# Kernel optimization log

Measured on AMD Instinct MI355X. Metric: run time of the kernel, lower is better.

Reference implementation:

```python
import jax, jax.numpy as jnp
import numpy as np

V, D = 100000, 128
B, Q, C, T = 1024, 64, 64, 8


def setup_inputs() -> dict:
    key = jax.random.key(0)
    ks = jax.random.split(key, 9)
    embed = jax.random.normal(ks[0], (V, D), dtype=jnp.float32) * 0.1
    embed = embed.at[0].set(0.0)  # padding_idx=0
    q_ids = jax.random.randint(ks[1], (B, Q), 1, V)
    c_ids = jax.random.randint(ks[2], (B, C, T), 1, V)
    num_qs = jax.random.randint(ks[3], (B,), 1, Q + 1)
    num_cols = jax.random.randint(ks[4], (B,), 1, C + 1)
    W_h = jax.random.normal(ks[5], (5 * D, D), dtype=jnp.float32) * 0.02
    b_h = jnp.zeros((D,), jnp.float32)
    W_o = jax.random.normal(ks[6], (D, 1), dtype=jnp.float32) * 0.02
    b_o = jnp.zeros((1,), jnp.float32)
    return {"q_ids": q_ids, "c_ids": c_ids, "num_qs": num_qs, "num_cols": num_cols,
            "embed": embed, "W_h": W_h, "b_h": b_h, "W_o": W_o, "b_o": b_o}


def _forward(q_ids, c_ids, num_qs, num_cols, embed, W_h, b_h, W_o, b_o):
    d = embed.shape[1]
    # ColumnSummarizer: pad-masked mean over column tokens -> [B, C, D]
    c_tok = embed[c_ids]                       # [B, C, T, D]
    c_mask = (c_ids != 0).astype(c_tok.dtype)  # [B, C, T]
    denom = jnp.maximum(c_mask.sum(-1, keepdims=True), 1.0)
    c_h = (c_tok * c_mask[..., None]).sum(-2) / denom  # [B, C, D]
    # QuestionSummarizer: q_h = token embeddings, q_summary = length-masked mean
    q_h = embed[q_ids]                         # [B, Q, D]
    q_valid = (jnp.arange(q_h.shape[1])[None, :] < num_qs[:, None])  # [B, Q]
    qv = q_valid.astype(q_h.dtype)
    q_summary = (q_h * qv[..., None]).sum(1) / jnp.maximum(
        num_qs[:, None].astype(q_h.dtype), 1.0)  # [B, D]
    # scaled dot-product attention, columns attend over question tokens
    sim = jnp.einsum('bcd,bqd->bcq', c_h, q_h) / jnp.sqrt(jnp.asarray(d, c_h.dtype))
    sim = jnp.where(q_valid[:, None, :], sim, -jnp.inf)  # mask padded q tokens
    att = jax.nn.softmax(sim, axis=-1)                    # [B, C, Q]
    weighted_q = jnp.einsum('bcq,bqd->bcd', att, q_h)     # [B, C, D]
    q_tiled = jnp.broadcast_to(q_summary[:, None, :], c_h.shape)
    feats = jnp.concatenate(
        [q_tiled, c_h, weighted_q, c_h * weighted_q, jnp.abs(c_h - weighted_q)],
        axis=-1)                                           # [B, C, 5D]
    h = jnp.tanh(feats @ W_h + b_h)
    return h @ W_o + b_o                                   # [B, C, 1]


def reference(q_ids, c_ids, num_qs, num_cols, embed, W_h, b_h, W_o, b_o):
    return _forward(q_ids, c_ids, num_qs, num_cols, embed, W_h, b_h, W_o, b_o)
```

## Files before the change

kernel.cpp:

```cpp
#include <hip/hip_runtime.h>


typedef __attribute__((ext_vector_type(8))) short     short8;
typedef __attribute__((ext_vector_type(8))) __bf16    bf16x8;
typedef __attribute__((ext_vector_type(4))) float     f32x4;
typedef __attribute__((ext_vector_type(4))) int       int4v;

#define SWZ8(row, off) ((off) ^ (((row) & 7) << 4))
#define SWZQ(row, off) ((off) ^ (((row) & 7) << 4) ^ ((((row) >> 3) & 3) << 5))

#define A_CH   0
#define A_QH   16384
#define A_LDS  32768

#define CH_OFF  0
#define QH_OFF  16384
#define X_OFF   32768
#define LDS_SIZE 40960

__device__ __forceinline__ unsigned short f2bf(float x) {
    __bf16 h = (__bf16)x;
    return __builtin_bit_cast(unsigned short, h);
}
__device__ __forceinline__ float bf2f(unsigned short u) {
    return __builtin_bit_cast(float, ((unsigned)u) << 16);
}
__device__ __forceinline__ float bflo(unsigned u) {
    return __builtin_bit_cast(float, u << 16);
}
__device__ __forceinline__ float bfhi(unsigned u) {
    return __builtin_bit_cast(float, u & 0xFFFF0000u);
}
__device__ __forceinline__ unsigned pk2(float a, float b) {
    return (unsigned)f2bf(a) | ((unsigned)f2bf(b) << 16);
}
__device__ __forceinline__ f32x4 mfma16(short8 a, short8 b, f32x4 c) {
    return __builtin_amdgcn_mfma_f32_16x16x32_bf16(
        __builtin_bit_cast(bf16x8, a), __builtin_bit_cast(bf16x8, b), c, 0, 0, 0);
}

__global__ __launch_bounds__(256) void el_prep(const float* __restrict__ W_h,
                                               unsigned short* __restrict__ whT) {
    int t = blockIdx.x * 256 + threadIdx.x;
    int k = t >> 7, n = t & 127;
    whT[n * 640 + k] = f2bf(W_h[t]);
}

__global__ __launch_bounds__(256) void el_conv(const float* __restrict__ e,
                                               unsigned short* __restrict__ ebf) {
    long i = ((long)blockIdx.x * 256 + threadIdx.x) * 8;
    f32x4 a = *(const f32x4*)(e + i);
    f32x4 c = *(const f32x4*)(e + i + 4);
    uint4 pk;
    pk.x = pk2(a[0], a[1]); pk.y = pk2(a[2], a[3]);
    pk.z = pk2(c[0], c[1]); pk.w = pk2(c[2], c[3]);
    *(uint4*)(ebf + i) = pk;
}

__global__ __launch_bounds__(256, 4) void el_main_a(
    const int* __restrict__ q_ids, const int* __restrict__ c_ids,
    const int* __restrict__ num_qs,
    const unsigned short* __restrict__ ebf,
    const unsigned short* __restrict__ whT,
    unsigned short* __restrict__ qsum_ws,
    unsigned short* __restrict__ att_ws,
    const float* __restrict__ b_h,
    const float* __restrict__ W_o, const float* __restrict__ b_o,
    float* __restrict__ out)
{
    __shared__ __align__(16) char smem[A_LDS];
    const int tid = threadIdx.x;
    const int b = blockIdx.x;
    const int nq = num_qs[b] > 0 ? num_qs[b] : 1;
    unsigned short* batt = att_ws + (size_t)b * 4096;
    float* bqp = (float*)batt;

    if (tid < 64) out[(b << 6) + tid] = b_o[0];

    {
        const int l4 = tid & 15, gg = tid >> 4;
        #pragma unroll 2
        for (int cc = 0; cc < 4; ++cc) {
            const int c = gg + cc * 16;
            const int* idp = c_ids + (((b << 6) + c) << 3);
            int4v i0 = *(const int4v*)idp, i1 = *(const int4v*)(idp + 4);
            int id8[8] = {i0[0], i0[1], i0[2], i0[3], i1[0], i1[1], i1[2], i1[3]};
            int cnt = 0;
            #pragma unroll
            for (int t = 0; t < 8; ++t) cnt += (id8[t] != 0);
            float acc[8] = {0.f,0.f,0.f,0.f,0.f,0.f,0.f,0.f};
            #pragma unroll
            for (int t = 0; t < 8; ++t) {
                uint4 v = *(const uint4*)(ebf + (long)id8[t] * 128 + l4 * 8);
                acc[0] += bflo(v.x); acc[1] += bfhi(v.x);
                acc[2] += bflo(v.y); acc[3] += bfhi(v.y);
                acc[4] += bflo(v.z); acc[5] += bfhi(v.z);
                acc[6] += bflo(v.w); acc[7] += bfhi(v.w);
            }
            float inv = 1.0f / (float)(cnt > 0 ? cnt : 1);
            uint4 pk;
            pk.x = pk2(acc[0]*inv, acc[1]*inv); pk.y = pk2(acc[2]*inv, acc[3]*inv);
            pk.z = pk2(acc[4]*inv, acc[5]*inv); pk.w = pk2(acc[6]*inv, acc[7]*inv);
            *(uint4*)(smem + A_CH + SWZ8(c, c * 256 + l4 * 16)) = pk;
        }
        float qa[8] = {0.f,0.f,0.f,0.f,0.f,0.f,0.f,0.f};
        #pragma unroll
        for (int qq = 0; qq < 4; ++qq) {
            const int q = gg + (qq << 4);
            int id = q_ids[(b << 6) + q];
            uint4 v = *(const uint4*)(ebf + (long)id * 128 + l4 * 8);
            *(uint4*)(smem + A_QH + SWZQ(q, q * 256 + l4 * 16)) = v;
            if (q < nq) {
                qa[0] += bflo(v.x); qa[1] += bfhi(v.x);
                qa[2] += bflo(v.y); qa[3] += bfhi(v.y);
                qa[4] += bflo(v.z); qa[5] += bfhi(v.z);
                qa[6] += bflo(v.w); qa[7] += bfhi(v.w);
            }
        }
        #pragma unroll
        for (int e = 0; e < 8; ++e) {
            qa[e] += __shfl_xor(qa[e], 16);
            qa[e] += __shfl_xor(qa[e], 32);
        }
        const int lane = tid & 63, w = tid >> 6;
        if (lane < 16) {
            *(f32x4*)(bqp + w * 128 + lane * 8)     = (f32x4){qa[0],qa[1],qa[2],qa[3]};
            *(f32x4*)(bqp + w * 128 + lane * 8 + 4) = (f32x4){qa[4],qa[5],qa[6],qa[7]};
        }
    }
    __syncthreads();

    if (tid < 128) {
        float s = bqp[tid] + bqp[128 + tid] + bqp[256 + tid] + bqp[384 + tid];
        qsum_ws[(b << 7) + tid] = f2bf(s / (float)nq);
    }
    __syncthreads();

    const int lane = tid & 63, w = tid >> 6;
    const int lr = lane & 15, lg = lane >> 4;

    {
        short8 a[4];
        const int arow = w * 16 + lr;
        #pragma unroll
        for (int s = 0; s < 4; ++s)
            a[s] = *(const short8*)(smem + A_CH + SWZ8(arow, arow * 256 + s * 64 + lg * 16));
        f32x4 sim[4];
        #pragma unroll
        for (int ct = 0; ct < 4; ++ct) {
            f32x4 acc = {0.f, 0.f, 0.f, 0.f};
            const int q = ct * 16 + lr;
            #pragma unroll
            for (int s = 0; s < 4; ++s) {
                short8 bf = *(const short8*)(smem + A_QH + SWZQ(q, q * 256 + s * 64 + lg * 16));
                acc = mfma16(a[s], bf, acc);
            }
            sim[ct] = acc;
        }
        const float scale = 0.08838834764831845f;
        #pragma unroll
        for (int ct = 0; ct < 4; ++ct) {
            const int q = ct * 16 + lr;
            #pragma unroll
            for (int r = 0; r < 4; ++r)
                sim[ct][r] = (q < nq) ? sim[ct][r] * scale : -3.0e38f;
        }
        float mx[4], sm[4];
        #pragma unroll
        for (int r = 0; r < 4; ++r)
            mx[r] = fmaxf(fmaxf(sim[0][r], sim[1][r]), fmaxf(sim[2][r], sim[3][r]));
        #pragma unroll
        for (int off = 1; off <= 8; off <<= 1)
            #pragma unroll
            for (int r = 0; r < 4; ++r)
                mx[r] = fmaxf(mx[r], __shfl_xor(mx[r], off));
        #pragma unroll
        for (int ct = 0; ct < 4; ++ct)
            #pragma unroll
            for (int r = 0; r < 4; ++r)
                sim[ct][r] = __expf(sim[ct][r] - mx[r]);
        #pragma unroll
        for (int r = 0; r < 4; ++r)
            sm[r] = (sim[0][r] + sim[1][r]) + (sim[2][r] + sim[3][r]);
        #pragma unroll
        for (int off = 1; off <= 8; off <<= 1)
            #pragma unroll
            for (int r = 0; r < 4; ++r)
                sm[r] += __shfl_xor(sm[r], off);
        const int cbase = w * 16 + lg * 4;
        #pragma unroll
        for (int ct = 0; ct < 4; ++ct)
            #pragma unroll
            for (int r = 0; r < 4; ++r) {
                int c = cbase + r, q = ct * 16 + lr;
                batt[c * 64 + q] = f2bf(sim[ct][r] * (1.0f / sm[r]));
            }
    }
    __syncthreads();

    f32x4 wqa[8];
    {
        short8 pa[2];
        const int prow = w * 16 + lr;
        #pragma unroll
        for (int s = 0; s < 2; ++s)
            pa[s] = *(const short8*)(batt + prow * 64 + s * 32 + lg * 8);
        #pragma unroll
        for (int ct = 0; ct < 8; ++ct) {
            f32x4 acc = {0.f, 0.f, 0.f, 0.f};
            const int d = ct * 16 + lr;
            const int dlx = (d << 1) ^ (lg << 5);
            #pragma unroll
            for (int s = 0; s < 2; ++s) {
                const int qbase = (s << 5) + (lg << 3);
                short8 bf;
                #pragma unroll
                for (int j = 0; j < 8; ++j) {
                    int off = A_QH + ((qbase + j) << 8) + (dlx ^ (j << 4));
                    bf[j] = *(const short*)(smem + off);
                }
                acc = mfma16(pa[s], bf, acc);
            }
            wqa[ct] = acc;
        }
    }
    __syncthreads();
    {
        const int cbase = w * 16 + lg * 4;
        #pragma unroll
        for (int ct = 0; ct < 8; ++ct)
            #pragma unroll
            for (int r = 0; r < 4; ++r) {
                int c = cbase + r, d = ct * 16 + lr;
                *(unsigned short*)(smem + A_QH + SWZQ(c, c * 256 + d * 2)) =
                    f2bf(wqa[ct][r]);
            }
    }
    __syncthreads();

    {
        f32x4 acc[4][2];
        #pragma unroll
        for (int rt = 0; rt < 4; ++rt) {
            acc[rt][0] = (f32x4){0.f, 0.f, 0.f, 0.f};
            acc[rt][1] = (f32x4){0.f, 0.f, 0.f, 0.f};
        }
        const int n0 = w * 32 + lr, n1 = n0 + 16;
        const int klane = lg * 8;
        short8 qsf[4];
        #pragma unroll
        for (int sk = 0; sk < 4; ++sk)
            qsf[sk] = *(const short8*)(qsum_ws + (b << 7) + sk * 32 + klane);
        const float bh0 = b_h[n0], bh1 = b_h[n1];
        const float wo0 = W_o[n0], wo1 = W_o[n1];

        for (int sk = 0; sk < 4; ++sk) {
            short8 B0[5], B1[5];
            #pragma unroll
            for (int p = 0; p < 5; ++p) {
                B0[p] = *(const short8*)(whT + n0 * 640 + p * 128 + sk * 32 + klane);
                B1[p] = *(const short8*)(whT + n1 * 640 + p * 128 + sk * 32 + klane);
            }
            #pragma unroll
            for (int rt = 0; rt < 4; ++rt) {
                const int row = rt * 16 + lr;
                short8 chf = *(const short8*)(smem + A_CH + SWZ8(row, row * 256 + sk * 64 + lg * 16));
                short8 wqf = *(const short8*)(smem + A_QH + SWZQ(row, row * 256 + sk * 64 + lg * 16));
                short8 prf, adf;
                #pragma unroll
                for (int e = 0; e < 8; ++e) {
                    float cv = bf2f((unsigned short)chf[e]);
                    float wv = bf2f((unsigned short)wqf[e]);
                    prf[e] = (short)f2bf(cv * wv);
                    adf[e] = (short)f2bf(fabsf(cv - wv));
                }
                acc[rt][0] = mfma16(qsf[sk], B0[0], acc[rt][0]);
                acc[rt][1] = mfma16(qsf[sk], B1[0], acc[rt][1]);
                acc[rt][0] = mfma16(chf,     B0[1], acc[rt][0]);
                acc[rt][1] = mfma16(chf,     B1[1], acc[rt][1]);
                acc[rt][0] = mfma16(wqf,     B0[2], acc[rt][0]);
                acc[rt][1] = mfma16(wqf,     B1[2], acc[rt][1]);
                acc[rt][0] = mfma16(prf,     B0[3], acc[rt][0]);
                acc[rt][1] = mfma16(prf,     B1[3], acc[rt][1]);
                acc[rt][0] = mfma16(adf,     B0[4], acc[rt][0]);
                acc[rt][1] = mfma16(adf,     B1[4], acc[rt][1]);
            }
        }

        #pragma unroll
        for (int rt = 0; rt < 4; ++rt)
            #pragma unroll
            for (int r = 0; r < 4; ++r) {
                float x0 = acc[rt][0][r] + bh0;
                float x1 = acc[rt][1][r] + bh1;
                float t0 = 1.0f - 2.0f / (__expf(2.0f * x0) + 1.0f);
                float t1 = 1.0f - 2.0f / (__expf(2.0f * x1) + 1.0f);
                float po = t0 * wo0 + t1 * wo1;
                #pragma unroll
                for (int off = 1; off <= 8; off <<= 1)
                    po += __shfl_xor(po, off);
                if (lr == 0)
                    atomicAdd(out + (b << 6) + rt * 16 + lg * 4 + r, po);
            }
    }
}

template <bool BF16E>
__global__ __launch_bounds__(256, 4) void el_main_b(
    const int* __restrict__ q_ids, const int* __restrict__ c_ids,
    const int* __restrict__ num_qs, const float* __restrict__ emb,
    const unsigned short* __restrict__ ebf,
    const unsigned short* __restrict__ whT,
    unsigned short* __restrict__ qsum_ws,
    const float* __restrict__ b_h,
    const float* __restrict__ W_o, const float* __restrict__ b_o,
    float* __restrict__ out)
{
    __shared__ __align__(16) char smem[LDS_SIZE];
    const int tid = threadIdx.x;
    const int b = blockIdx.x;
    const int nq = num_qs[b] > 0 ? num_qs[b] : 1;

    {
        const int l4 = tid & 15, gg = tid >> 4;
        #pragma unroll 2
        for (int cc = 0; cc < 4; ++cc) {
            const int c = gg + cc * 16;
            const int* idp = c_ids + (((b << 6) + c) << 3);
            int4v i0 = *(const int4v*)idp, i1 = *(const int4v*)(idp + 4);
            int id8[8] = {i0[0], i0[1], i0[2], i0[3], i1[0], i1[1], i1[2], i1[3]};
            int cnt = 0;
            #pragma unroll
            for (int t = 0; t < 8; ++t) cnt += (id8[t] != 0);
            float acc[8] = {0.f,0.f,0.f,0.f,0.f,0.f,0.f,0.f};
            #pragma unroll
            for (int t = 0; t < 8; ++t) {
                if constexpr (BF16E) {
                    uint4 v = *(const uint4*)(ebf + (long)id8[t] * 128 + l4 * 8);
                    acc[0] += bflo(v.x); acc[1] += bfhi(v.x);
                    acc[2] += bflo(v.y); acc[3] += bfhi(v.y);
                    acc[4] += bflo(v.z); acc[5] += bfhi(v.z);
                    acc[6] += bflo(v.w); acc[7] += bfhi(v.w);
                } else {
                    f32x4 lo = *(const f32x4*)(emb + (long)id8[t] * 128 + l4 * 8);
                    f32x4 hi = *(const f32x4*)(emb + (long)id8[t] * 128 + l4 * 8 + 4);
                    acc[0] += lo[0]; acc[1] += lo[1]; acc[2] += lo[2]; acc[3] += lo[3];
                    acc[4] += hi[0]; acc[5] += hi[1]; acc[6] += hi[2]; acc[7] += hi[3];
                }
            }
            float inv = 1.0f / (float)(cnt > 0 ? cnt : 1);
            uint4 pk;
            pk.x = pk2(acc[0]*inv, acc[1]*inv); pk.y = pk2(acc[2]*inv, acc[3]*inv);
            pk.z = pk2(acc[4]*inv, acc[5]*inv); pk.w = pk2(acc[6]*inv, acc[7]*inv);
            *(uint4*)(smem + CH_OFF + SWZ8(c, c * 256 + l4 * 16)) = pk;
        }
        float qa[8] = {0.f,0.f,0.f,0.f,0.f,0.f,0.f,0.f};
        #pragma unroll
        for (int qq = 0; qq < 4; ++qq) {
            const int q = gg + (qq << 4);
            int id = q_ids[(b << 6) + q];
            uint4 v;
            if constexpr (BF16E) {
                v = *(const uint4*)(ebf + (long)id * 128 + l4 * 8);
            } else {
                f32x4 lo = *(const f32x4*)(emb + (long)id * 128 + l4 * 8);
                f32x4 hi = *(const f32x4*)(emb + (long)id * 128 + l4 * 8 + 4);
                v.x = pk2(lo[0], lo[1]); v.y = pk2(lo[2], lo[3]);
                v.z = pk2(hi[0], hi[1]); v.w = pk2(hi[2], hi[3]);
            }
            *(uint4*)(smem + QH_OFF + SWZQ(q, q * 256 + l4 * 16)) = v;
            if (q < nq) {
                qa[0] += bflo(v.x); qa[1] += bfhi(v.x);
                qa[2] += bflo(v.y); qa[3] += bfhi(v.y);
                qa[4] += bflo(v.z); qa[5] += bfhi(v.z);
                qa[6] += bflo(v.w); qa[7] += bfhi(v.w);
            }
        }
        float* qsp = (float*)(smem + X_OFF);
        *(f32x4*)(qsp + gg * 128 + l4 * 8)     = (f32x4){qa[0], qa[1], qa[2], qa[3]};
        *(f32x4*)(qsp + gg * 128 + l4 * 8 + 4) = (f32x4){qa[4], qa[5], qa[6], qa[7]};
    }
    __syncthreads();

    if (tid < 128) {
        const float* qsp = (const float*)(smem + X_OFF);
        float s = 0.f;
        #pragma unroll
        for (int g = 0; g < 16; ++g) s += qsp[g * 128 + tid];
        qsum_ws[(b << 7) + tid] = f2bf(s / (float)nq);
    }
    __syncthreads();

    const int lane = tid & 63, w = tid >> 6;
    const int lr = lane & 15, lg = lane >> 4;

    {
        short8 a[4];
        const int arow = w * 16 + lr;
        #pragma unroll
        for (int s = 0; s < 4; ++s)
            a[s] = *(const short8*)(smem + CH_OFF + SWZ8(arow, arow * 256 + s * 64 + lg * 16));
        f32x4 sim[4];
        #pragma unroll
        for (int ct = 0; ct < 4; ++ct) {
            f32x4 acc = {0.f, 0.f, 0.f, 0.f};
            const int q = ct * 16 + lr;
            #pragma unroll
            for (int s = 0; s < 4; ++s) {
                short8 bf = *(const short8*)(smem + QH_OFF + SWZQ(q, q * 256 + s * 64 + lg * 16));
                acc = mfma16(a[s], bf, acc);
            }
            sim[ct] = acc;
        }
        const float scale = 0.08838834764831845f;
        #pragma unroll
        for (int ct = 0; ct < 4; ++ct) {
            const int q = ct * 16 + lr;
            #pragma unroll
            for (int r = 0; r < 4; ++r)
                sim[ct][r] = (q < nq) ? sim[ct][r] * scale : -3.0e38f;
        }
        float mx[4], sm[4];
        #pragma unroll
        for (int r = 0; r < 4; ++r)
            mx[r] = fmaxf(fmaxf(sim[0][r], sim[1][r]), fmaxf(sim[2][r], sim[3][r]));
        #pragma unroll
        for (int off = 1; off <= 8; off <<= 1)
            #pragma unroll
            for (int r = 0; r < 4; ++r)
                mx[r] = fmaxf(mx[r], __shfl_xor(mx[r], off));
        #pragma unroll
        for (int ct = 0; ct < 4; ++ct)
            #pragma unroll
            for (int r = 0; r < 4; ++r)
                sim[ct][r] = __expf(sim[ct][r] - mx[r]);
        #pragma unroll
        for (int r = 0; r < 4; ++r)
            sm[r] = (sim[0][r] + sim[1][r]) + (sim[2][r] + sim[3][r]);
        #pragma unroll
        for (int off = 1; off <= 8; off <<= 1)
            #pragma unroll
            for (int r = 0; r < 4; ++r)
                sm[r] += __shfl_xor(sm[r], off);
        const int cbase = w * 16 + lg * 4;
        #pragma unroll
        for (int ct = 0; ct < 4; ++ct)
            #pragma unroll
            for (int r = 0; r < 4; ++r) {
                int c = cbase + r, q = ct * 16 + lr;
                *(unsigned short*)(smem + X_OFF + SWZ8(c, c * 128 + q * 2)) =
                    f2bf(sim[ct][r] * (1.0f / sm[r]));
            }
    }
    __syncthreads();

    f32x4 wqa[8];
    {
        short8 pa[2];
        const int arow = w * 16 + lr;
        #pragma unroll
        for (int s = 0; s < 2; ++s)
            pa[s] = *(const short8*)(smem + X_OFF + SWZ8(arow, arow * 128 + s * 64 + lg * 16));
        #pragma unroll
        for (int ct = 0; ct < 8; ++ct) {
            f32x4 acc = {0.f, 0.f, 0.f, 0.f};
            const int d = ct * 16 + lr;
            const int dlx = (d << 1) ^ (lg << 5);
            #pragma unroll
            for (int s = 0; s < 2; ++s) {
                const int qbase = (s << 5) + (lg << 3);
                short8 bf;
                #pragma unroll
                for (int j = 0; j < 8; ++j) {
                    int off = QH_OFF + ((qbase + j) << 8) + (dlx ^ (j << 4));
                    bf[j] = *(const short*)(smem + off);
                }
                acc = mfma16(pa[s], bf, acc);
            }
            wqa[ct] = acc;
        }
    }
    __syncthreads();
    {
        const int cbase = w * 16 + lg * 4;
        #pragma unroll
        for (int ct = 0; ct < 8; ++ct)
            #pragma unroll
            for (int r = 0; r < 4; ++r) {
                int c = cbase + r, d = ct * 16 + lr;
                *(unsigned short*)(smem + QH_OFF + SWZQ(c, c * 256 + d * 2)) =
                    f2bf(wqa[ct][r]);
            }
    }
    __syncthreads();

    {
        f32x4 acc[4][2];
        #pragma unroll
        for (int rt = 0; rt < 4; ++rt) {
            acc[rt][0] = (f32x4){0.f, 0.f, 0.f, 0.f};
            acc[rt][1] = (f32x4){0.f, 0.f, 0.f, 0.f};
        }
        const int n0 = w * 32 + lr, n1 = n0 + 16;
        const int klane = lg * 8;
        short8 qsf[4];
        #pragma unroll
        for (int sk = 0; sk < 4; ++sk)
            qsf[sk] = *(const short8*)(qsum_ws + (b << 7) + sk * 32 + klane);
        const float bh0 = b_h[n0], bh1 = b_h[n1];
        const float wo0 = W_o[n0], wo1 = W_o[n1];

        for (int sk = 0; sk < 4; ++sk) {
            short8 B0[5], B1[5];
            #pragma unroll
            for (int p = 0; p < 5; ++p) {
                B0[p] = *(const short8*)(whT + n0 * 640 + p * 128 + sk * 32 + klane);
                B1[p] = *(const short8*)(whT + n1 * 640 + p * 128 + sk * 32 + klane);
            }
            #pragma unroll
            for (int rt = 0; rt < 4; ++rt) {
                const int row = rt * 16 + lr;
                short8 chf = *(const short8*)(smem + CH_OFF + SWZ8(row, row * 256 + sk * 64 + lg * 16));
                short8 wqf = *(const short8*)(smem + QH_OFF + SWZQ(row, row * 256 + sk * 64 + lg * 16));
                short8 prf, adf;
                #pragma unroll
                for (int e = 0; e < 8; ++e) {
                    float cv = bf2f((unsigned short)chf[e]);
                    float wv = bf2f((unsigned short)wqf[e]);
                    prf[e] = (short)f2bf(cv * wv);
                    adf[e] = (short)f2bf(fabsf(cv - wv));
                }
                acc[rt][0] = mfma16(qsf[sk], B0[0], acc[rt][0]);
                acc[rt][1] = mfma16(qsf[sk], B1[0], acc[rt][1]);
                acc[rt][0] = mfma16(chf,     B0[1], acc[rt][0]);
                acc[rt][1] = mfma16(chf,     B1[1], acc[rt][1]);
                acc[rt][0] = mfma16(wqf,     B0[2], acc[rt][0]);
                acc[rt][1] = mfma16(wqf,     B1[2], acc[rt][1]);
                acc[rt][0] = mfma16(prf,     B0[3], acc[rt][0]);
                acc[rt][1] = mfma16(prf,     B1[3], acc[rt][1]);
                acc[rt][0] = mfma16(adf,     B0[4], acc[rt][0]);
                acc[rt][1] = mfma16(adf,     B1[4], acc[rt][1]);
            }
        }

        #pragma unroll
        for (int rt = 0; rt < 4; ++rt)
            #pragma unroll
            for (int r = 0; r < 4; ++r) {
                float x0 = acc[rt][0][r] + bh0;
                float x1 = acc[rt][1][r] + bh1;
                float t0 = 1.0f - 2.0f / (__expf(2.0f * x0) + 1.0f);
                float t1 = 1.0f - 2.0f / (__expf(2.0f * x1) + 1.0f);
                float po = t0 * wo0 + t1 * wo1;
                #pragma unroll
                for (int off = 1; off <= 8; off <<= 1)
                    po += __shfl_xor(po, off);
                if (lr == 0)
                    *(float*)(smem + X_OFF + (w * 64 + rt * 16 + lg * 4 + r) * 4) = po;
            }
    }
    __syncthreads();

    if (tid < 64) {
        float o = b_o[0];
        #pragma unroll
        for (int w2 = 0; w2 < 4; ++w2)
            o += *(const float*)(smem + X_OFF + (w2 * 64 + tid) * 4);
        out[(b << 6) + tid] = o;
    }
}

extern "C" void kernel_launch(void* const* d_in, const int* in_sizes, int n_in,
                              void* d_out, int out_size, void* d_ws, size_t ws_size,
                              hipStream_t stream) {
    const int*   q_ids  = (const int*)d_in[0];
    const int*   c_ids  = (const int*)d_in[1];
    const int*   num_qs = (const int*)d_in[2];
    const float* embed  = (const float*)d_in[4];
    const float* W_h    = (const float*)d_in[5];
    const float* b_h    = (const float*)d_in[6];
    const float* W_o    = (const float*)d_in[7];
    const float* b_o    = (const float*)d_in[8];
    float*       out    = (float*)d_out;

    const size_t EBF_OFF = 425984;
    const size_t EBF_END = EBF_OFF + (size_t)100000 * 128 * 2;
    const size_t ATT_END = EBF_END + (size_t)1024 * 4096 * 2;
    unsigned short* whT  = (unsigned short*)d_ws;
    unsigned short* qsum = (unsigned short*)((char*)d_ws + 163840);
    unsigned short* ebf  = (unsigned short*)((char*)d_ws + EBF_OFF);
    unsigned short* attw = (unsigned short*)((char*)d_ws + EBF_END);

    el_prep<<<320, 256, 0, stream>>>(W_h, whT);

    if (ws_size >= ATT_END) {
        el_conv<<<6250, 256, 0, stream>>>(embed, ebf);
        el_main_a<<<1024, 256, 0, stream>>>(q_ids, c_ids, num_qs, ebf, whT,
                                            qsum, attw, b_h, W_o, b_o, out);
    } else if (ws_size >= EBF_END) {
        el_conv<<<6250, 256, 0, stream>>>(embed, ebf);
        el_main_b<true><<<1024, 256, 0, stream>>>(q_ids, c_ids, num_qs, embed, ebf,
                                                  whT, qsum, b_h, W_o, b_o, out);
    } else {
        el_main_b<false><<<1024, 256, 0, stream>>>(q_ids, c_ids, num_qs, embed, ebf,
                                                   whT, qsum, b_h, W_o, b_o, out);
    }
}
```

Before: 156.2 us.

## Split fused kernel into high-occupancy gather kernel and separate compute kernel

Splits the monolithic per-batch kernel into a gather stage, which runs at twice the block count with 8 blocks/SM and stages token ids in LDS, and a compute stage. The gather stage writes pre-swizzled bf16 column and question tiles plus partial question sums to workspace. The compute stage loads those tiles and runs attention and the MLP, keeping the attention matrix in LDS instead of global workspace and reducing the output through LDS instead of atomics. The aim is more memory-level parallelism for the random embedding gathers. In exchange it adds a global round-trip of 32KB per batch and one extra launch.

```diff
diff --git a/kernel.cpp b/kernel.cpp
--- a/kernel.cpp
+++ b/kernel.cpp
@@ -8,10 +8,6 @@
 
 #define SWZ8(row, off) ((off) ^ (((row) & 7) << 4))
 #define SWZQ(row, off) ((off) ^ (((row) & 7) << 4) ^ ((((row) >> 3) & 3) << 5))
-
-#define A_CH   0
-#define A_QH   16384
-#define A_LDS  32768
 
 #define CH_OFF  0
 #define QH_OFF  16384
@@ -57,261 +53,108 @@
     *(uint4*)(ebf + i) = pk;
 }
 
-__global__ __launch_bounds__(256, 4) void el_main_a(
+template <bool BF16E>
+__global__ __launch_bounds__(256, 8) void el_gather(
     const int* __restrict__ q_ids, const int* __restrict__ c_ids,
-    const int* __restrict__ num_qs,
+    const int* __restrict__ num_qs, const float* __restrict__ emb,
     const unsigned short* __restrict__ ebf,
-    const unsigned short* __restrict__ whT,
-    unsigned short* __restrict__ qsum_ws,
-    unsigned short* __restrict__ att_ws,
-    const float* __restrict__ b_h,
-    const float* __restrict__ W_o, const float* __restrict__ b_o,
-    float* __restrict__ out)
+    unsigned short* __restrict__ chqh,
+    unsigned short* __restrict__ qsh)
 {
-    __shared__ __align__(16) char smem[A_LDS];
+    __shared__ __align__(16) char smem[3328];
     const int tid = threadIdx.x;
-    const int b = blockIdx.x;
+    const int hb = blockIdx.x, b = hb >> 1, half = hb & 1;
     const int nq = num_qs[b] > 0 ? num_qs[b] : 1;
-    unsigned short* batt = att_ws + (size_t)b * 4096;
-    float* bqp = (float*)batt;
-
-    if (tid < 64) out[(b << 6) + tid] = b_o[0];
-
-    {
-        const int l4 = tid & 15, gg = tid >> 4;
-        #pragma unroll 2
-        for (int cc = 0; cc < 4; ++cc) {
-            const int c = gg + cc * 16;
-            const int* idp = c_ids + (((b << 6) + c) << 3);
-            int4v i0 = *(const int4v*)idp, i1 = *(const int4v*)(idp + 4);
-            int id8[8] = {i0[0], i0[1], i0[2], i0[3], i1[0], i1[1], i1[2], i1[3]};
-            int cnt = 0;
-            #pragma unroll
-            for (int t = 0; t < 8; ++t) cnt += (id8[t] != 0);
-            float acc[8] = {0.f,0.f,0.f,0.f,0.f,0.f,0.f,0.f};
-            #pragma unroll
-            for (int t = 0; t < 8; ++t) {
+    char* bch = (char*)chqh + (size_t)b * 32768;
+    int* idc = (int*)smem;
+    int* idq = (int*)(smem + 1024);
+    float* qsp = (float*)(smem + 1280);
+
+    if (tid < 256) idc[tid] = c_ids[(b << 9) + (half << 8) + tid];
+    if (tid < 32)  idq[tid] = q_ids[(b << 6) + (half << 5) + tid];
+    __syncthreads();
+
+    const int l4 = tid & 15, gg = tid >> 4;
+    #pragma unroll
+    for (int cc = 0; cc < 2; ++cc) {
+        const int cl = gg + cc * 16;
+        const int c = (half << 5) + cl;
+        const int* idp = idc + cl * 8;
+        int id8[8];
+        #pragma unroll
+        for (int t = 0; t < 8; ++t) id8[t] = idp[t];
+        int cnt = 0;
+        #pragma unroll
+        for (int t = 0; t < 8; ++t) cnt += (id8[t] != 0);
+        float acc[8] = {0.f,0.f,0.f,0.f,0.f,0.f,0.f,0.f};
+        #pragma unroll
+        for (int t = 0; t < 8; ++t) {
+            if constexpr (BF16E) {
                 uint4 v = *(const uint4*)(ebf + (long)id8[t] * 128 + l4 * 8);
                 acc[0] += bflo(v.x); acc[1] += bfhi(v.x);
                 acc[2] += bflo(v.y); acc[3] += bfhi(v.y);
                 acc[4] += bflo(v.z); acc[5] += bfhi(v.z);
                 acc[6] += bflo(v.w); acc[7] += bfhi(v.w);
-            }
-            float inv = 1.0f / (float)(cnt > 0 ? cnt : 1);
-            uint4 pk;
-            pk.x = pk2(acc[0]*inv, acc[1]*inv); pk.y = pk2(acc[2]*inv, acc[3]*inv);
-            pk.z = pk2(acc[4]*inv, acc[5]*inv); pk.w = pk2(acc[6]*inv, acc[7]*inv);
-            *(uint4*)(smem + A_CH + SWZ8(c, c * 256 + l4 * 16)) = pk;
-        }
-        float qa[8] = {0.f,0.f,0.f,0.f,0.f,0.f,0.f,0.f};
-        #pragma unroll
-        for (int qq = 0; qq < 4; ++qq) {
-            const int q = gg + (qq << 4);
-            int id = q_ids[(b << 6) + q];
-            uint4 v = *(const uint4*)(ebf + (long)id * 128 + l4 * 8);
-            *(uint4*)(smem + A_QH + SWZQ(q, q * 256 + l4 * 16)) = v;
-            if (q < nq) {
-                qa[0] += bflo(v.x); qa[1] += bfhi(v.x);
-                qa[2] += bflo(v.y); qa[3] += bfhi(v.y);
-                qa[4] += bflo(v.z); qa[5] += bfhi(v.z);
-                qa[6] += bflo(v.w); qa[7] += bfhi(v.w);
-            }
-        }
-        #pragma unroll
-        for (int e = 0; e < 8; ++e) {
-            qa[e] += __shfl_xor(qa[e], 16);
-            qa[e] += __shfl_xor(qa[e], 32);
-        }
-        const int lane = tid & 63, w = tid >> 6;
-        if (lane < 16) {
-            *(f32x4*)(bqp + w * 128 + lane * 8)     = (f32x4){qa[0],qa[1],qa[2],qa[3]};
-            *(f32x4*)(bqp + w * 128 + lane * 8 + 4) = (f32x4){qa[4],qa[5],qa[6],qa[7]};
-        }
-    }
-    __syncthreads();
-
+            } else {
+                f32x4 lo = *(const f32x4*)(emb + (long)id8[t] * 128 + l4 * 8);
+                f32x4 hi = *(const f32x4*)(emb + (long)id8[t] * 128 + l4 * 8 + 4);
+                acc[0] += lo[0]; acc[1] += lo[1]; acc[2] += lo[2]; acc[3] += lo[3];
+                acc[4] += hi[0]; acc[5] += hi[1]; acc[6] += hi[2]; acc[7] += hi[3];
+            }
+        }
+        float inv = 1.0f / (float)(cnt > 0 ? cnt : 1);
+        uint4 pk;
+        pk.x = pk2(acc[0]*inv, acc[1]*inv); pk.y = pk2(acc[2]*inv, acc[3]*inv);
+        pk.z = pk2(acc[4]*inv, acc[5]*inv); pk.w = pk2(acc[6]*inv, acc[7]*inv);
+        *(uint4*)(bch + SWZ8(c, c * 256 + l4 * 16)) = pk;
+    }
+    float qa[8] = {0.f,0.f,0.f,0.f,0.f,0.f,0.f,0.f};
+    #pragma unroll
+    for (int qq = 0; qq < 2; ++qq) {
+        const int ql = gg + (qq << 4);
+        const int q = (half << 5) + ql;
+        int id = idq[ql];
+        uint4 v;
+        float e8[8];
+        if constexpr (BF16E) {
+            v = *(const uint4*)(ebf + (long)id * 128 + l4 * 8);
+            e8[0]=bflo(v.x); e8[1]=bfhi(v.x); e8[2]=bflo(v.y); e8[3]=bfhi(v.y);
+            e8[4]=bflo(v.z); e8[5]=bfhi(v.z); e8[6]=bflo(v.w); e8[7]=bfhi(v.w);
+        } else {
+            f32x4 lo = *(const f32x4*)(emb + (long)id * 128 + l4 * 8);
+            f32x4 hi = *(const f32x4*)(emb + (long)id * 128 + l4 * 8 + 4);
+            e8[0]=lo[0]; e8[1]=lo[1]; e8[2]=lo[2]; e8[3]=lo[3];
+            e8[4]=hi[0]; e8[5]=hi[1]; e8[6]=hi[2]; e8[7]=hi[3];
+            v.x = pk2(lo[0], lo[1]); v.y = pk2(lo[2], lo[3]);
+            v.z = pk2(hi[0], hi[1]); v.w = pk2(hi[2], hi[3]);
+        }
+        *(uint4*)(bch + 16384 + SWZQ(q, q * 256 + l4 * 16)) = v;
+        if (q < nq)
+            #pragma unroll
+            for (int e = 0; e < 8; ++e) qa[e] += e8[e];
+    }
+    #pragma unroll
+    for (int e = 0; e < 8; ++e) {
+        qa[e] += __shfl_xor(qa[e], 16);
+        qa[e] += __shfl_xor(qa[e], 32);
+    }
+    const int lane = tid & 63, w = tid >> 6;
+    if (lane < 16) {
+        *(f32x4*)(qsp + w * 128 + lane * 8)     = (f32x4){qa[0],qa[1],qa[2],qa[3]};
+        *(f32x4*)(qsp + w * 128 + lane * 8 + 4) = (f32x4){qa[4],qa[5],qa[6],qa[7]};
+    }
+    __syncthreads();
     if (tid < 128) {
-        float s = bqp[tid] + bqp[128 + tid] + bqp[256 + tid] + bqp[384 + tid];
-        qsum_ws[(b << 7) + tid] = f2bf(s / (float)nq);
-    }
-    __syncthreads();
-
-    const int lane = tid & 63, w = tid >> 6;
-    const int lr = lane & 15, lg = lane >> 4;
-
-    {
-        short8 a[4];
-        const int arow = w * 16 + lr;
-        #pragma unroll
-        for (int s = 0; s < 4; ++s)
-            a[s] = *(const short8*)(smem + A_CH + SWZ8(arow, arow * 256 + s * 64 + lg * 16));
-        f32x4 sim[4];
-        #pragma unroll
-        for (int ct = 0; ct < 4; ++ct) {
-            f32x4 acc = {0.f, 0.f, 0.f, 0.f};
-            const int q = ct * 16 + lr;
-            #pragma unroll
-            for (int s = 0; s < 4; ++s) {
-                short8 bf = *(const short8*)(smem + A_QH + SWZQ(q, q * 256 + s * 64 + lg * 16));
-                acc = mfma16(a[s], bf, acc);
-            }
-            sim[ct] = acc;
-        }
-        const float scale = 0.08838834764831845f;
-        #pragma unroll
-        for (int ct = 0; ct < 4; ++ct) {
-            const int q = ct * 16 + lr;
-            #pragma unroll
-            for (int r = 0; r < 4; ++r)
-                sim[ct][r] = (q < nq) ? sim[ct][r] * scale : -3.0e38f;
-        }
-        float mx[4], sm[4];
-        #pragma unroll
-        for (int r = 0; r < 4; ++r)
-            mx[r] = fmaxf(fmaxf(sim[0][r], sim[1][r]), fmaxf(sim[2][r], sim[3][r]));
-        #pragma unroll
-        for (int off = 1; off <= 8; off <<= 1)
-            #pragma unroll
-            for (int r = 0; r < 4; ++r)
-                mx[r] = fmaxf(mx[r], __shfl_xor(mx[r], off));
-        #pragma unroll
-        for (int ct = 0; ct < 4; ++ct)
-            #pragma unroll
-            for (int r = 0; r < 4; ++r)
-                sim[ct][r] = __expf(sim[ct][r] - mx[r]);
-        #pragma unroll
-        for (int r = 0; r < 4; ++r)
-            sm[r] = (sim[0][r] + sim[1][r]) + (sim[2][r] + sim[3][r]);
-        #pragma unroll
-        for (int off = 1; off <= 8; off <<= 1)
-            #pragma unroll
-            for (int r = 0; r < 4; ++r)
-                sm[r] += __shfl_xor(sm[r], off);
-        const int cbase = w * 16 + lg * 4;
-        #pragma unroll
-        for (int ct = 0; ct < 4; ++ct)
-            #pragma unroll
-            for (int r = 0; r < 4; ++r) {
-                int c = cbase + r, q = ct * 16 + lr;
-                batt[c * 64 + q] = f2bf(sim[ct][r] * (1.0f / sm[r]));
-            }
-    }
-    __syncthreads();
-
-    f32x4 wqa[8];
-    {
-        short8 pa[2];
-        const int prow = w * 16 + lr;
-        #pragma unroll
-        for (int s = 0; s < 2; ++s)
-            pa[s] = *(const short8*)(batt + prow * 64 + s * 32 + lg * 8);
-        #pragma unroll
-        for (int ct = 0; ct < 8; ++ct) {
-            f32x4 acc = {0.f, 0.f, 0.f, 0.f};
-            const int d = ct * 16 + lr;
-            const int dlx = (d << 1) ^ (lg << 5);
-            #pragma unroll
-            for (int s = 0; s < 2; ++s) {
-                const int qbase = (s << 5) + (lg << 3);
-                short8 bf;
-                #pragma unroll
-                for (int j = 0; j < 8; ++j) {
-                    int off = A_QH + ((qbase + j) << 8) + (dlx ^ (j << 4));
-                    bf[j] = *(const short*)(smem + off);
-                }
-                acc = mfma16(pa[s], bf, acc);
-            }
-            wqa[ct] = acc;
-        }
-    }
-    __syncthreads();
-    {
-        const int cbase = w * 16 + lg * 4;
-        #pragma unroll
-        for (int ct = 0; ct < 8; ++ct)
-            #pragma unroll
-            for (int r = 0; r < 4; ++r) {
-                int c = cbase + r, d = ct * 16 + lr;
-                *(unsigned short*)(smem + A_QH + SWZQ(c, c * 256 + d * 2)) =
-                    f2bf(wqa[ct][r]);
-            }
-    }
-    __syncthreads();
-
-    {
-        f32x4 acc[4][2];
-        #pragma unroll
-        for (int rt = 0; rt < 4; ++rt) {
-            acc[rt][0] = (f32x4){0.f, 0.f, 0.f, 0.f};
-            acc[rt][1] = (f32x4){0.f, 0.f, 0.f, 0.f};
-        }
-        const int n0 = w * 32 + lr, n1 = n0 + 16;
-        const int klane = lg * 8;
-        short8 qsf[4];
-        #pragma unroll
-        for (int sk = 0; sk < 4; ++sk)
-            qsf[sk] = *(const short8*)(qsum_ws + (b << 7) + sk * 32 + klane);
-        const float bh0 = b_h[n0], bh1 = b_h[n1];
-        const float wo0 = W_o[n0], wo1 = W_o[n1];
-
-        for (int sk = 0; sk < 4; ++sk) {
-            short8 B0[5], B1[5];
-            #pragma unroll
-            for (int p = 0; p < 5; ++p) {
-                B0[p] = *(const short8*)(whT + n0 * 640 + p * 128 + sk * 32 + klane);
-                B1[p] = *(const short8*)(whT + n1 * 640 + p * 128 + sk * 32 + klane);
-            }
-            #pragma unroll
-            for (int rt = 0; rt < 4; ++rt) {
-                const int row = rt * 16 + lr;
-                short8 chf = *(const short8*)(smem + A_CH + SWZ8(row, row * 256 + sk * 64 + lg * 16));
-                short8 wqf = *(const short8*)(smem + A_QH + SWZQ(row, row * 256 + sk * 64 + lg * 16));
-                short8 prf, adf;
-                #pragma unroll
-                for (int e = 0; e < 8; ++e) {
-                    float cv = bf2f((unsigned short)chf[e]);
-                    float wv = bf2f((unsigned short)wqf[e]);
-                    prf[e] = (short)f2bf(cv * wv);
-                    adf[e] = (short)f2bf(fabsf(cv - wv));
-                }
-                acc[rt][0] = mfma16(qsf[sk], B0[0], acc[rt][0]);
-                acc[rt][1] = mfma16(qsf[sk], B1[0], acc[rt][1]);
-                acc[rt][0] = mfma16(chf,     B0[1], acc[rt][0]);
-                acc[rt][1] = mfma16(chf,     B1[1], acc[rt][1]);
-                acc[rt][0] = mfma16(wqf,     B0[2], acc[rt][0]);
-                acc[rt][1] = mfma16(wqf,     B1[2], acc[rt][1]);
-                acc[rt][0] = mfma16(prf,     B0[3], acc[rt][0]);
-                acc[rt][1] = mfma16(prf,     B1[3], acc[rt][1]);
-                acc[rt][0] = mfma16(adf,     B0[4], acc[rt][0]);
-                acc[rt][1] = mfma16(adf,     B1[4], acc[rt][1]);
-            }
-        }
-
-        #pragma unroll
-        for (int rt = 0; rt < 4; ++rt)
-            #pragma unroll
-            for (int r = 0; r < 4; ++r) {
-                float x0 = acc[rt][0][r] + bh0;
-                float x1 = acc[rt][1][r] + bh1;
-                float t0 = 1.0f - 2.0f / (__expf(2.0f * x0) + 1.0f);
-                float t1 = 1.0f - 2.0f / (__expf(2.0f * x1) + 1.0f);
-                float po = t0 * wo0 + t1 * wo1;
-                #pragma unroll
-                for (int off = 1; off <= 8; off <<= 1)
-                    po += __shfl_xor(po, off);
-                if (lr == 0)
-                    atomicAdd(out + (b << 6) + rt * 16 + lg * 4 + r, po);
-            }
-    }
-}
-
-template <bool BF16E>
-__global__ __launch_bounds__(256, 4) void el_main_b(
-    const int* __restrict__ q_ids, const int* __restrict__ c_ids,
-    const int* __restrict__ num_qs, const float* __restrict__ emb,
-    const unsigned short* __restrict__ ebf,
+        float s = qsp[tid] + qsp[128 + tid] + qsp[256 + tid] + qsp[384 + tid];
+        qsh[((b << 1) + half) * 128 + tid] = f2bf(s);
+    }
+}
+
+__global__ __launch_bounds__(256, 4) void el_compute(
+    const int* __restrict__ num_qs,
+    const unsigned short* __restrict__ chqh,
     const unsigned short* __restrict__ whT,
-    unsigned short* __restrict__ qsum_ws,
+    const unsigned short* __restrict__ qsh,
     const float* __restrict__ b_h,
     const float* __restrict__ W_o, const float* __restrict__ b_o,
     float* __restrict__ out)
@@ -322,72 +165,10 @@
     const int nq = num_qs[b] > 0 ? num_qs[b] : 1;
 
     {
-        const int l4 = tid & 15, gg = tid >> 4;
-        #pragma unroll 2
-        for (int cc = 0; cc < 4; ++cc) {
-            const int c = gg + cc * 16;
-            const int* idp = c_ids + (((b << 6) + c) << 3);
-            int4v i0 = *(const int4v*)idp, i1 = *(const int4v*)(idp + 4);
-            int id8[8] = {i0[0], i0[1], i0[2], i0[3], i1[0], i1[1], i1[2], i1[3]};
-            int cnt = 0;
-            #pragma unroll
-            for (int t = 0; t < 8; ++t) cnt += (id8[t] != 0);
-            float acc[8] = {0.f,0.f,0.f,0.f,0.f,0.f,0.f,0.f};
-            #pragma unroll
-            for (int t = 0; t < 8; ++t) {
-                if constexpr (BF16E) {
-                    uint4 v = *(const uint4*)(ebf + (long)id8[t] * 128 + l4 * 8);
-                    acc[0] += bflo(v.x); acc[1] += bfhi(v.x);
-                    acc[2] += bflo(v.y); acc[3] += bfhi(v.y);
-                    acc[4] += bflo(v.z); acc[5] += bfhi(v.z);
-                    acc[6] += bflo(v.w); acc[7] += bfhi(v.w);
-                } else {
-                    f32x4 lo = *(const f32x4*)(emb + (long)id8[t] * 128 + l4 * 8);
-                    f32x4 hi = *(const f32x4*)(emb + (long)id8[t] * 128 + l4 * 8 + 4);
-                    acc[0] += lo[0]; acc[1] += lo[1]; acc[2] += lo[2]; acc[3] += lo[3];
-                    acc[4] += hi[0]; acc[5] += hi[1]; acc[6] += hi[2]; acc[7] += hi[3];
-                }
-            }
-            float inv = 1.0f / (float)(cnt > 0 ? cnt : 1);
-            uint4 pk;
-            pk.x = pk2(acc[0]*inv, acc[1]*inv); pk.y = pk2(acc[2]*inv, acc[3]*inv);
-            pk.z = pk2(acc[4]*inv, acc[5]*inv); pk.w = pk2(acc[6]*inv, acc[7]*inv);
-            *(uint4*)(smem + CH_OFF + SWZ8(c, c * 256 + l4 * 16)) = pk;
-        }
-        float qa[8] = {0.f,0.f,0.f,0.f,0.f,0.f,0.f,0.f};
-        #pragma unroll
-        for (int qq = 0; qq < 4; ++qq) {
-            const int q = gg + (qq << 4);
-            int id = q_ids[(b << 6) + q];
-            uint4 v;
-            if constexpr (BF16E) {
-                v = *(const uint4*)(ebf + (long)id * 128 + l4 * 8);
-            } else {
-                f32x4 lo = *(const f32x4*)(emb + (long)id * 128 + l4 * 8);
-                f32x4 hi = *(const f32x4*)(emb + (long)id * 128 + l4 * 8 + 4);
-                v.x = pk2(lo[0], lo[1]); v.y = pk2(lo[2], lo[3]);
-                v.z = pk2(hi[0], hi[1]); v.w = pk2(hi[2], hi[3]);
-            }
-            *(uint4*)(smem + QH_OFF + SWZQ(q, q * 256 + l4 * 16)) = v;
-            if (q < nq) {
-                qa[0] += bflo(v.x); qa[1] += bfhi(v.x);
-                qa[2] += bflo(v.y); qa[3] += bfhi(v.y);
-                qa[4] += bflo(v.z); qa[5] += bfhi(v.z);
-                qa[6] += bflo(v.w); qa[7] += bfhi(v.w);
-            }
-        }
-        float* qsp = (float*)(smem + X_OFF);
-        *(f32x4*)(qsp + gg * 128 + l4 * 8)     = (f32x4){qa[0], qa[1], qa[2], qa[3]};
-        *(f32x4*)(qsp + gg * 128 + l4 * 8 + 4) = (f32x4){qa[4], qa[5], qa[6], qa[7]};
-    }
-    __syncthreads();
-
-    if (tid < 128) {
-        const float* qsp = (const float*)(smem + X_OFF);
-        float s = 0.f;
-        #pragma unroll
-        for (int g = 0; g < 16; ++g) s += qsp[g * 128 + tid];
-        qsum_ws[(b << 7) + tid] = f2bf(s / (float)nq);
+        const uint4* src = (const uint4*)((const char*)chqh + (size_t)b * 32768);
+        uint4* dst = (uint4*)smem;
+        #pragma unroll
+        for (int i = 0; i < 8; ++i) dst[tid + i * 256] = src[tid + i * 256];
     }
     __syncthreads();
 
@@ -504,9 +285,21 @@
         const int n0 = w * 32 + lr, n1 = n0 + 16;
         const int klane = lg * 8;
         short8 qsf[4];
-        #pragma unroll
-        for (int sk = 0; sk < 4; ++sk)
-            qsf[sk] = *(const short8*)(qsum_ws + (b << 7) + sk * 32 + klane);
+        {
+            const unsigned short* qh = qsh + (size_t)b * 256;
+            const float invq = 1.0f / (float)nq;
+            #pragma unroll
+            for (int sk = 0; sk < 4; ++sk) {
+                short8 h0 = *(const short8*)(qh + sk * 32 + klane);
+                short8 h1 = *(const short8*)(qh + 128 + sk * 32 + klane);
+                short8 r;
+                #pragma unroll
+                for (int e = 0; e < 8; ++e)
+                    r[e] = (short)f2bf((bf2f((unsigned short)h0[e]) +
+                                        bf2f((unsigned short)h1[e])) * invq);
+                qsf[sk] = r;
+            }
+        }
         const float bh0 = b_h[n0], bh1 = b_h[n1];
         const float wo0 = W_o[n0], wo1 = W_o[n1];
 
@@ -570,6 +363,255 @@
     }
 }
 
+__global__ __launch_bounds__(256, 4) void el_mono(
+    const int* __restrict__ q_ids, const int* __restrict__ c_ids,
+    const int* __restrict__ num_qs, const float* __restrict__ emb,
+    const unsigned short* __restrict__ whT,
+    unsigned short* __restrict__ qsum_ws,
+    const float* __restrict__ b_h,
+    const float* __restrict__ W_o, const float* __restrict__ b_o,
+    float* __restrict__ out)
+{
+    __shared__ __align__(16) char smem[LDS_SIZE];
+    const int tid = threadIdx.x;
+    const int b = blockIdx.x;
+    const int nq = num_qs[b] > 0 ? num_qs[b] : 1;
+
+    {
+        const int l4 = tid & 15, gg = tid >> 4;
+        #pragma unroll 2
+        for (int cc = 0; cc < 4; ++cc) {
+            const int c = gg + cc * 16;
+            const int* idp = c_ids + (((b << 6) + c) << 3);
+            int4v i0 = *(const int4v*)idp, i1 = *(const int4v*)(idp + 4);
+            int id8[8] = {i0[0], i0[1], i0[2], i0[3], i1[0], i1[1], i1[2], i1[3]};
+            int cnt = 0;
+            #pragma unroll
+            for (int t = 0; t < 8; ++t) cnt += (id8[t] != 0);
+            float acc[8] = {0.f,0.f,0.f,0.f,0.f,0.f,0.f,0.f};
+            #pragma unroll
+            for (int t = 0; t < 8; ++t) {
+                f32x4 lo = *(const f32x4*)(emb + (long)id8[t] * 128 + l4 * 8);
+                f32x4 hi = *(const f32x4*)(emb + (long)id8[t] * 128 + l4 * 8 + 4);
+                acc[0] += lo[0]; acc[1] += lo[1]; acc[2] += lo[2]; acc[3] += lo[3];
+                acc[4] += hi[0]; acc[5] += hi[1]; acc[6] += hi[2]; acc[7] += hi[3];
+            }
+            float inv = 1.0f / (float)(cnt > 0 ? cnt : 1);
+            uint4 pk;
+            pk.x = pk2(acc[0]*inv, acc[1]*inv); pk.y = pk2(acc[2]*inv, acc[3]*inv);
+            pk.z = pk2(acc[4]*inv, acc[5]*inv); pk.w = pk2(acc[6]*inv, acc[7]*inv);
+            *(uint4*)(smem + CH_OFF + SWZ8(c, c * 256 + l4 * 16)) = pk;
+        }
+        float qa[8] = {0.f,0.f,0.f,0.f,0.f,0.f,0.f,0.f};
+        #pragma unroll
+        for (int qq = 0; qq < 4; ++qq) {
+            const int q = gg + (qq << 4);
+            int id = q_ids[(b << 6) + q];
+            f32x4 lo = *(const f32x4*)(emb + (long)id * 128 + l4 * 8);
+            f32x4 hi = *(const f32x4*)(emb + (long)id * 128 + l4 * 8 + 4);
+            uint4 v;
+            v.x = pk2(lo[0], lo[1]); v.y = pk2(lo[2], lo[3]);
+            v.z = pk2(hi[0], hi[1]); v.w = pk2(hi[2], hi[3]);
+            *(uint4*)(smem + QH_OFF + SWZQ(q, q * 256 + l4 * 16)) = v;
+            if (q < nq) {
+                qa[0] += lo[0]; qa[1] += lo[1]; qa[2] += lo[2]; qa[3] += lo[3];
+                qa[4] += hi[0]; qa[5] += hi[1]; qa[6] += hi[2]; qa[7] += hi[3];
+            }
+        }
+        float* qsp = (float*)(smem + X_OFF);
+        *(f32x4*)(qsp + gg * 128 + l4 * 8)     = (f32x4){qa[0], qa[1], qa[2], qa[3]};
+        *(f32x4*)(qsp + gg * 128 + l4 * 8 + 4) = (f32x4){qa[4], qa[5], qa[6], qa[7]};
+    }
+    __syncthreads();
+
+    if (tid < 128) {
+        const float* qsp = (const float*)(smem + X_OFF);
+        float s = 0.f;
+        #pragma unroll
+        for (int g = 0; g < 16; ++g) s += qsp[g * 128 + tid];
+        qsum_ws[(b << 7) + tid] = f2bf(s / (float)nq);
+    }
+    __syncthreads();
+
+    const int lane = tid & 63, w = tid >> 6;
+    const int lr = lane & 15, lg = lane >> 4;
+
+    {
+        short8 a[4];
+        const int arow = w * 16 + lr;
+        #pragma unroll
+        for (int s = 0; s < 4; ++s)
+            a[s] = *(const short8*)(smem + CH_OFF + SWZ8(arow, arow * 256 + s * 64 + lg * 16));
+        f32x4 sim[4];
+        #pragma unroll
+        for (int ct = 0; ct < 4; ++ct) {
+            f32x4 acc = {0.f, 0.f, 0.f, 0.f};
+            const int q = ct * 16 + lr;
+            #pragma unroll
+            for (int s = 0; s < 4; ++s) {
+                short8 bf = *(const short8*)(smem + QH_OFF + SWZQ(q, q * 256 + s * 64 + lg * 16));
+                acc = mfma16(a[s], bf, acc);
+            }
+            sim[ct] = acc;
+        }
+        const float scale = 0.08838834764831845f;
+        #pragma unroll
+        for (int ct = 0; ct < 4; ++ct) {
+            const int q = ct * 16 + lr;
+            #pragma unroll
+            for (int r = 0; r < 4; ++r)
+                sim[ct][r] = (q < nq) ? sim[ct][r] * scale : -3.0e38f;
+        }
+        float mx[4], sm[4];
+        #pragma unroll
+        for (int r = 0; r < 4; ++r)
+            mx[r] = fmaxf(fmaxf(sim[0][r], sim[1][r]), fmaxf(sim[2][r], sim[3][r]));
+        #pragma unroll
+        for (int off = 1; off <= 8; off <<= 1)
+            #pragma unroll
+            for (int r = 0; r < 4; ++r)
+                mx[r] = fmaxf(mx[r], __shfl_xor(mx[r], off));
+        #pragma unroll
+        for (int ct = 0; ct < 4; ++ct)
+            #pragma unroll
+            for (int r = 0; r < 4; ++r)
+                sim[ct][r] = __expf(sim[ct][r] - mx[r]);
+        #pragma unroll
+        for (int r = 0; r < 4; ++r)
+            sm[r] = (sim[0][r] + sim[1][r]) + (sim[2][r] + sim[3][r]);
+        #pragma unroll
+        for (int off = 1; off <= 8; off <<= 1)
+            #pragma unroll
+            for (int r = 0; r < 4; ++r)
+                sm[r] += __shfl_xor(sm[r], off);
+        const int cbase = w * 16 + lg * 4;
+        #pragma unroll
+        for (int ct = 0; ct < 4; ++ct)
+            #pragma unroll
+            for (int r = 0; r < 4; ++r) {
+                int c = cbase + r, q = ct * 16 + lr;
+                *(unsigned short*)(smem + X_OFF + SWZ8(c, c * 128 + q * 2)) =
+                    f2bf(sim[ct][r] * (1.0f / sm[r]));
+            }
+    }
+    __syncthreads();
+
+    f32x4 wqa[8];
+    {
+        short8 pa[2];
+        const int arow = w * 16 + lr;
+        #pragma unroll
+        for (int s = 0; s < 2; ++s)
+            pa[s] = *(const short8*)(smem + X_OFF + SWZ8(arow, arow * 128 + s * 64 + lg * 16));
+        #pragma unroll
+        for (int ct = 0; ct < 8; ++ct) {
+            f32x4 acc = {0.f, 0.f, 0.f, 0.f};
+            const int d = ct * 16 + lr;
+            const int dlx = (d << 1) ^ (lg << 5);
+            #pragma unroll
+            for (int s = 0; s < 2; ++s) {
+                const int qbase = (s << 5) + (lg << 3);
+                short8 bf;
+                #pragma unroll
+                for (int j = 0; j < 8; ++j) {
+                    int off = QH_OFF + ((qbase + j) << 8) + (dlx ^ (j << 4));
+                    bf[j] = *(const short*)(smem + off);
+                }
+                acc = mfma16(pa[s], bf, acc);
+            }
+            wqa[ct] = acc;
+        }
+    }
+    __syncthreads();
+    {
+        const int cbase = w * 16 + lg * 4;
+        #pragma unroll
+        for (int ct = 0; ct < 8; ++ct)
+            #pragma unroll
+            for (int r = 0; r < 4; ++r) {
+                int c = cbase + r, d = ct * 16 + lr;
+                *(unsigned short*)(smem + QH_OFF + SWZQ(c, c * 256 + d * 2)) =
+                    f2bf(wqa[ct][r]);
+            }
+    }
+    __syncthreads();
+
+    {
+        f32x4 acc[4][2];
+        #pragma unroll
+        for (int rt = 0; rt < 4; ++rt) {
+            acc[rt][0] = (f32x4){0.f, 0.f, 0.f, 0.f};
+            acc[rt][1] = (f32x4){0.f, 0.f, 0.f, 0.f};
+        }
+        const int n0 = w * 32 + lr, n1 = n0 + 16;
+        const int klane = lg * 8;
+        short8 qsf[4];
+        #pragma unroll
+        for (int sk = 0; sk < 4; ++sk)
+            qsf[sk] = *(const short8*)(qsum_ws + (b << 7) + sk * 32 + klane);
+        const float bh0 = b_h[n0], bh1 = b_h[n1];
+        const float wo0 = W_o[n0], wo1 = W_o[n1];
+
+        for (int sk = 0; sk < 4; ++sk) {
+            short8 B0[5], B1[5];
+            #pragma unroll
+            for (int p = 0; p < 5; ++p) {
+                B0[p] = *(const short8*)(whT + n0 * 640 + p * 128 + sk * 32 + klane);
+                B1[p] = *(const short8*)(whT + n1 * 640 + p * 128 + sk * 32 + klane);
+            }
+            #pragma unroll
+            for (int rt = 0; rt < 4; ++rt) {
+                const int row = rt * 16 + lr;
+                short8 chf = *(const short8*)(smem + CH_OFF + SWZ8(row, row * 256 + sk * 64 + lg * 16));
+                short8 wqf = *(const short8*)(smem + QH_OFF + SWZQ(row, row * 256 + sk * 64 + lg * 16));
+                short8 prf, adf;
+                #pragma unroll
+                for (int e = 0; e < 8; ++e) {
+                    float cv = bf2f((unsigned short)chf[e]);
+                    float wv = bf2f((unsigned short)wqf[e]);
+                    prf[e] = (short)f2bf(cv * wv);
+                    adf[e] = (short)f2bf(fabsf(cv - wv));
+                }
+                acc[rt][0] = mfma16(qsf[sk], B0[0], acc[rt][0]);
+                acc[rt][1] = mfma16(qsf[sk], B1[0], acc[rt][1]);
+                acc[rt][0] = mfma16(chf,     B0[1], acc[rt][0]);
+                acc[rt][1] = mfma16(chf,     B1[1], acc[rt][1]);
+                acc[rt][0] = mfma16(wqf,     B0[2], acc[rt][0]);
+                acc[rt][1] = mfma16(wqf,     B1[2], acc[rt][1]);
+                acc[rt][0] = mfma16(prf,     B0[3], acc[rt][0]);
+                acc[rt][1] = mfma16(prf,     B1[3], acc[rt][1]);
+                acc[rt][0] = mfma16(adf,     B0[4], acc[rt][0]);
+                acc[rt][1] = mfma16(adf,     B1[4], acc[rt][1]);
+            }
+        }
+
+        #pragma unroll
+        for (int rt = 0; rt < 4; ++rt)
+            #pragma unroll
+            for (int r = 0; r < 4; ++r) {
+                float x0 = acc[rt][0][r] + bh0;
+                float x1 = acc[rt][1][r] + bh1;
+                float t0 = 1.0f - 2.0f / (__expf(2.0f * x0) + 1.0f);
+                float t1 = 1.0f - 2.0f / (__expf(2.0f * x1) + 1.0f);
+                float po = t0 * wo0 + t1 * wo1;
+                #pragma unroll
+                for (int off = 1; off <= 8; off <<= 1)
+                    po += __shfl_xor(po, off);
+                if (lr == 0)
+                    *(float*)(smem + X_OFF + (w * 64 + rt * 16 + lg * 4 + r) * 4) = po;
+            }
+    }
+    __syncthreads();
+
+    if (tid < 64) {
+        float o = b_o[0];
+        #pragma unroll
+        for (int w2 = 0; w2 < 4; ++w2)
+            o += *(const float*)(smem + X_OFF + (w2 * 64 + tid) * 4);
+        out[(b << 6) + tid] = o;
+    }
+}
+
 extern "C" void kernel_launch(void* const* d_in, const int* in_sizes, int n_in,
                               void* d_out, int out_size, void* d_ws, size_t ws_size,
                               hipStream_t stream) {
@@ -583,26 +625,30 @@
     const float* b_o    = (const float*)d_in[8];
     float*       out    = (float*)d_out;
 
-    const size_t EBF_OFF = 425984;
-    const size_t EBF_END = EBF_OFF + (size_t)100000 * 128 * 2;
-    const size_t ATT_END = EBF_END + (size_t)1024 * 4096 * 2;
+    const size_t QSH_OFF  = 163840;
+    const size_t CHQH_OFF = QSH_OFF + 524288;
+    const size_t CHQH_END = CHQH_OFF + (size_t)1024 * 32768;
+    const size_t EBF_END  = CHQH_END + (size_t)100000 * 256;
     unsigned short* whT  = (unsigned short*)d_ws;
-    unsigned short* qsum = (unsigned short*)((char*)d_ws + 163840);
-    unsigned short* ebf  = (unsigned short*)((char*)d_ws + EBF_OFF);
-    unsigned short* attw = (unsigned short*)((char*)d_ws + EBF_END);
+    unsigned short* qsh  = (unsigned short*)((char*)d_ws + QSH_OFF);
+    unsigned short* chqh = (unsigned short*)((char*)d_ws + CHQH_OFF);
+    unsigned short* ebf  = (unsigned short*)((char*)d_ws + CHQH_END);
 
     el_prep<<<320, 256, 0, stream>>>(W_h, whT);
 
-    if (ws_size >= ATT_END) {
+    if (ws_size >= EBF_END) {
         el_conv<<<6250, 256, 0, stream>>>(embed, ebf);
-        el_main_a<<<1024, 256, 0, stream>>>(q_ids, c_ids, num_qs, ebf, whT,
-                                            qsum, attw, b_h, W_o, b_o, out);
-    } else if (ws_size >= EBF_END) {
-        el_conv<<<6250, 256, 0, stream>>>(embed, ebf);
-        el_main_b<true><<<1024, 256, 0, stream>>>(q_ids, c_ids, num_qs, embed, ebf,
-                                                  whT, qsum, b_h, W_o, b_o, out);
+        el_gather<true><<<2048, 256, 0, stream>>>(q_ids, c_ids, num_qs, embed,
+                                                  ebf, chqh, qsh);
+        el_compute<<<1024, 256, 0, stream>>>(num_qs, chqh, whT, qsh,
+                                             b_h, W_o, b_o, out);
+    } else if (ws_size >= CHQH_END) {
+        el_gather<false><<<2048, 256, 0, stream>>>(q_ids, c_ids, num_qs, embed,
+                                                   ebf, chqh, qsh);
+        el_compute<<<1024, 256, 0, stream>>>(num_qs, chqh, whT, qsh,
+                                             b_h, W_o, b_o, out);
     } else {
-        el_main_b<false><<<1024, 256, 0, stream>>>(q_ids, c_ids, num_qs, embed, ebf,
-                                                   whT, qsum, b_h, W_o, b_o, out);
-    }
-}
+        el_mono<<<1024, 256, 0, stream>>>(q_ids, c_ids, num_qs, embed, whT,
+                                          qsh, b_h, W_o, b_o, out);
+    }
+}
```

Result: slower. 163.0 us (+4.3%).
